# Performance work log

Hardware: AMD Instinct MI355X
Metric: run time of the kernel (lower is better)

The kernel has to match this reference:

```python
import jax, jax.numpy as jnp
import numpy as np

NEG = -1e9  # finite stand-in for -inf (avoids inf-inf NaNs, safe in fp32)


def setup_inputs() -> dict:
    T, V, Lmax, A = 2048, 8192, 8, 64
    rng = np.random.default_rng(0)
    seq = rng.integers(0, A, size=T).astype(np.int32)
    # first A pieces are the single codepoints -> every sequence is segmentable
    piece_lens = np.concatenate([
        np.ones(A, np.int32),
        rng.integers(1, Lmax + 1, size=V - A).astype(np.int32),
    ])
    pieces = rng.integers(0, A, size=(V, Lmax)).astype(np.int32)
    pieces[:A, 0] = np.arange(A)
    logits = rng.standard_normal(V).astype(np.float32)
    m = logits.max()
    log_probs = (logits - m - np.log(np.exp(logits - m).sum())).astype(np.float32)
    return {
        'seq': jnp.asarray(seq),
        'pieces': jnp.asarray(pieces),
        'piece_lens': jnp.asarray(piece_lens),
        'log_probs': jnp.asarray(log_probs),
    }


def reference(seq, pieces, piece_lens, log_probs):
    T = seq.shape[0]
    V, Lmax = pieces.shape
    dt = log_probs.dtype

    # --- match table: match[t, i] = piece i matches sequence at position t ---
    seq_pad = jnp.concatenate([seq, jnp.full((Lmax,), -1, seq.dtype)])
    windows = seq_pad[jnp.arange(T)[:, None] + jnp.arange(Lmax)[None, :]]  # [T, Lmax]
    lmask = jnp.arange(Lmax)[None, :] < piece_lens[:, None]                # [V, Lmax]
    eq = windows[:, None, :] == pieces[None, :, :]                        # [T, V, Lmax]
    fits = (jnp.arange(T)[:, None] + piece_lens[None, :]) <= T            # [T, V]
    match = jnp.all(eq | ~lmask[None, :, :], axis=-1) & fits              # [T, V]
    mlp = jnp.where(match, log_probs[None, :], NEG).astype(dt)            # [T, V]

    # end_logp[t-1, i] = mlp[t - len_i, i]  (piece i ending exactly at t, t=1..T)
    te = jnp.arange(1, T + 1)[:, None]
    src = te - piece_lens[None, :]
    end_logp = jnp.where(src >= 0,
                         mlp[jnp.clip(src, 0, T - 1), jnp.arange(V)[None, :]],
                         NEG)

    # --- forward pass: alpha[t] = logsumexp_i alpha[t - len_i] + log p_i ---
    idx_a = Lmax - piece_lens  # window slot holding alpha[t - len_i]
    def fstep(win, row):
        a_t = jax.nn.logsumexp(win[idx_a] + row)
        return jnp.concatenate([win[1:], a_t[None]]), a_t
    win0 = jnp.full((Lmax,), NEG, dt).at[-1].set(0.0)
    _, alpha_rest = jax.lax.scan(fstep, win0, end_logp)
    alpha = jnp.concatenate([jnp.zeros((1,), dt), alpha_rest])  # [T+1]

    # --- backward pass: beta[t] = logsumexp_i log p_i + beta[t + len_i] ---
    idx_b = piece_lens - 1  # window slot holding beta[t + len_i]
    def bstep(win, row):
        b_t = jax.nn.logsumexp(row + win[idx_b])
        return jnp.concatenate([b_t[None], win[:-1]]), b_t
    winT = jnp.full((Lmax,), NEG, dt).at[0].set(0.0)
    _, beta_rev = jax.lax.scan(bstep, winT, mlp[::-1])
    beta = jnp.concatenate([beta_rev[::-1], jnp.zeros((1,), dt)])  # [T+1]

    # --- posteriors: P[t, i] = exp(alpha[t] + log p_i + beta[t+len_i] - alpha[T]) ---
    norm = alpha[T]
    beta_next = beta[jnp.clip(jnp.arange(T)[:, None] + piece_lens[None, :], 0, T)]
    P = jnp.exp(alpha[:T][:, None] + mlp + beta_next - norm)
    P = jnp.where(match, P, 0.0)
    return jnp.where(norm > NEG / 2, P, jnp.zeros_like(P))
```

## Files before the change

### kernel.cpp

```cpp
#include <hip/hip_runtime.h>
#include <stdint.h>

#define LMAX 8
#define KCH 32
#define NC  64
#define TT  2048
#define LN2D 0.6931471805599453
#define NEGE (-(1<<28))

struct __align__(16) PK { unsigned long long key; float logp; int len; };

__device__ __forceinline__ int fexp(float m) { return ((__float_as_int(m) >> 23) & 0xFF) - 127; }
__device__ __forceinline__ int fexpbits(float m) { return (__float_as_int(m) >> 23) & 0xFF; }
__device__ __forceinline__ float p2(int e) { return __int_as_float((e + 127) << 23); }
__device__ __forceinline__ float p2c(int e) { return (e < -126) ? 0.f : p2(e); }

__global__ void k_prep(const int* __restrict__ seq, const int* __restrict__ pieces,
                       const int* __restrict__ plens, const float* __restrict__ logp,
                       PK* __restrict__ pk, unsigned long long* __restrict__ w64,
                       float* __restrict__ M, int T, int V) {
  int idx = blockIdx.x * blockDim.x + threadIdx.x;
  if (idx < V) {
    const int* pr = pieces + idx * LMAX;
    int len = plens[idx];
    unsigned long long key = 0ull;
    #pragma unroll
    for (int l = 0; l < LMAX; ++l) {
      unsigned long long b = (unsigned long long)(pr[l] & 0xFF);
      if (l < len) key |= b << (8 * l);
    }
    PK o; o.key = key; o.logp = logp[idx]; o.len = len;
    pk[idx] = o;
  } else if (idx < V + T) {
    int t = idx - V;
    unsigned long long w = 0ull;
    #pragma unroll
    for (int l = 0; l < LMAX; ++l) {
      int pos = t + l;
      unsigned long long b = (pos < T) ? (unsigned long long)(seq[pos] & 0xFF) : 0xFFull;
      w |= b << (8 * l);
    }
    w64[t] = w;
  } else if (idx < V + T + T * LMAX) {
    M[idx - V - T] = 0.f;
  }
}

__global__ void k_match(const PK* __restrict__ pk, const unsigned long long* __restrict__ w64,
                        float* __restrict__ M, int T, int V, int tPer) {
  int v = blockIdx.x * blockDim.x + threadIdx.x;
  PK p = pk[v];
  unsigned long long mask = (p.len >= 8) ? ~0ull : ((1ull << (8 * p.len)) - 1ull);
  unsigned long long key = p.key;
  int t0 = blockIdx.y * tPer;
  float prob = -1.f;
  for (int t = t0; t < t0 + tPer; ++t) {
    unsigned long long w = w64[t];
    if (((w ^ key) & mask) == 0ull) {
      if (prob < 0.f) prob = expf(p.logp);
      atomicAdd(&M[t * LMAX + (p.len - 1)], prob);
    }
  }
}

__global__ __launch_bounds__(512) void k_scan(const float* __restrict__ M,
        float* __restrict__ Wt, float* __restrict__ P,
        double* __restrict__ aD, double* __restrict__ bD,
        float* __restrict__ aL, float* __restrict__ bL) {
  __shared__ float  Gm[2 * 8 * 69];
  __shared__ float  Cs[2 * 64 * 9];
  __shared__ float  Sg[2 * 8 * 9];
  __shared__ int    EWc[2 * 64 * 8];
  __shared__ int    EPs[2 * 64 * 8];
  __shared__ int    EGs[2 * 8 * 8];
  __shared__ int    EaccP[2 * 64];
  __shared__ int    EsB[2 * 8];
  const int tid = threadIdx.x;
  const float4* Mv = (const float4*)M;

  {
    const int dir = tid >> 8, lt = tid & 255;
    const int c = lt >> 2, h = lt & 3;
    const int base = c * KCH;
    float st[2][8];
    #pragma unroll
    for (int bb = 0; bb < 2; ++bb)
      #pragma unroll
      for (int i = 0; i < 8; ++i) st[bb][i] = (i == 2 * h + bb) ? p2(64) : 0.f;
    int ec = -64;
    if (dir == 0) {
      float4 ra = Mv[base * 2], rb = Mv[base * 2 + 1];
      for (int kg = 0; kg < 4; ++kg) {
        #pragma unroll
        for (int kk = 0; kk < 8; ++kk) {
          int k = kg * 8 + kk;
          float4 c0 = ra, c1 = rb;
          int nk = (k + 1 < KCH) ? k + 1 : KCH - 1;
          ra = Mv[(base + nk) * 2]; rb = Mv[(base + nk) * 2 + 1];
          #pragma unroll
          for (int bb = 0; bb < 2; ++bb) {
            float a_ = st[bb][kk & 7];
            st[bb][(kk + 1) & 7] = fmaf(a_, c0.x, st[bb][(kk + 1) & 7]);
            st[bb][(kk + 2) & 7] = fmaf(a_, c0.y, st[bb][(kk + 2) & 7]);
            st[bb][(kk + 3) & 7] = fmaf(a_, c0.z, st[bb][(kk + 3) & 7]);
            st[bb][(kk + 4) & 7] = fmaf(a_, c0.w, st[bb][(kk + 4) & 7]);
            st[bb][(kk + 5) & 7] = fmaf(a_, c1.x, st[bb][(kk + 5) & 7]);
            st[bb][(kk + 6) & 7] = fmaf(a_, c1.y, st[bb][(kk + 6) & 7]);
            st[bb][(kk + 7) & 7] = fmaf(a_, c1.z, st[bb][(kk + 7) & 7]);
            st[bb][kk & 7]       = a_ * c1.w;
          }
          if (kk == 3 || kk == 7) {
            float mx = 0.f;
            #pragma unroll
            for (int bb = 0; bb < 2; ++bb)
              #pragma unroll
              for (int i = 0; i < 8; ++i) mx = fmaxf(mx, st[bb][i]);
            if (fexpbits(mx) != 0) {
              int e = fexp(mx), d = 64 - e;
              float m1 = p2(d / 2), m2 = p2(d - d / 2);
              #pragma unroll
              for (int bb = 0; bb < 2; ++bb)
                #pragma unroll
                for (int i = 0; i < 8; ++i) st[bb][i] = st[bb][i] * m1 * m2;
              ec += e - 64;
            }
          }
        }
      }
    } else {
      float4 ra = Mv[(base + KCH - 1) * 2], rb = Mv[(base + KCH - 1) * 2 + 1];
      for (int kg = 0; kg < 4; ++kg) {
        #pragma unroll
        for (int kk = 0; kk < 8; ++kk) {
          int k = kg * 8 + kk;
          float4 c0 = ra, c1 = rb;
          int nk = (k + 1 < KCH) ? k + 1 : KCH - 1;
          int nt = base + KCH - 1 - nk;
          ra = Mv[nt * 2]; rb = Mv[nt * 2 + 1];
          #pragma unroll
          for (int bb = 0; bb < 2; ++bb) {
            float nb =      c0.x * st[bb][(8  - kk) & 7];
            nb = fmaf(c0.y, st[bb][(9  - kk) & 7], nb);
            nb = fmaf(c0.z, st[bb][(10 - kk) & 7], nb);
            nb = fmaf(c0.w, st[bb][(11 - kk) & 7], nb);
            nb = fmaf(c1.x, st[bb][(12 - kk) & 7], nb);
            nb = fmaf(c1.y, st[bb][(13 - kk) & 7], nb);
            nb = fmaf(c1.z, st[bb][(14 - kk) & 7], nb);
            nb = fmaf(c1.w, st[bb][(15 - kk) & 7], nb);
            st[bb][(7 - kk) & 7] = nb;
          }
          if (kk == 3 || kk == 7) {
            float mx = 0.f;
            #pragma unroll
            for (int bb = 0; bb < 2; ++bb)
              #pragma unroll
              for (int i = 0; i < 8; ++i) mx = fmaxf(mx, st[bb][i]);
            if (fexpbits(mx) != 0) {
              int e = fexp(mx), d = 64 - e;
              float m1 = p2(d / 2), m2 = p2(d - d / 2);
              #pragma unroll
              for (int bb = 0; bb < 2; ++bb)
                #pragma unroll
                for (int i = 0; i < 8; ++i) st[bb][i] = st[bb][i] * m1 * m2;
              ec += e - 64;
            }
          }
        }
      }
    }
    float mx = 0.f;
    #pragma unroll
    for (int bb = 0; bb < 2; ++bb)
      #pragma unroll
      for (int i = 0; i < 8; ++i) mx = fmaxf(mx, st[bb][i]);
    int lc = dir ? (NC - 1 - c) : c;
    float* wp = Wt + (dir * 64 + lc) * 68;
    int ew;
    if (fexpbits(mx) == 0) {
      ew = NEGE;
      #pragma unroll
      for (int bb = 0; bb < 2; ++bb)
        #pragma unroll
        for (int i = 0; i < 8; ++i) wp[(2 * h + bb) * 8 + i] = 0.f;
    } else {
      int e = fexp(mx);
      float sc = p2(-e);
      ew = ec + e;
      #pragma unroll
      for (int bb = 0; bb < 2; ++bb)
        #pragma unroll
        for (int i = 0; i < 8; ++i) wp[(2 * h + bb) * 8 + i] = st[bb][i] * sc;
    }
    EWc[(dir * 64 + lc) * 8 + 2 * h]     = ew;
    EWc[(dir * 64 + lc) * 8 + 2 * h + 1] = ew;
  }
  __syncthreads();

  if (tid < 128) {
    const int dir = tid >> 6, w = (tid >> 3) & 7, b = tid & 7;
    float v[8];
    #pragma unroll
    for (int i = 0; i < 8; ++i) v[i] = (i == b) ? 1.f : 0.f;
    int ec = 0;
    for (int c = 0; c < 8; ++c) {
      int lc = w * 8 + c;
      float* pp = P + (dir * 64 + lc) * 69 + b * 8;
      #pragma unroll
      for (int i = 0; i < 8; ++i) pp[i] = v[i];
      EPs[(dir * 64 + lc) * 8 + b] = ec;
      const float* wp = Wt + (dir * 64 + lc) * 68;
      int ew[8];
      #pragma unroll
      for (int j = 0; j < 8; ++j) ew[j] = EWc[(dir * 64 + lc) * 8 + j];
      int emax = ew[0];
      #pragma unroll
      for (int j = 1; j < 8; ++j) emax = max(emax, ew[j]);
      float nv[8] = {0, 0, 0, 0, 0, 0, 0, 0};
      #pragma unroll
      for (int j = 0; j < 8; ++j) {
        float tj = v[j] * p2c(ew[j] - emax + 64);
        float4 ca = *(const float4*)(wp + j * 8);
        float4 cb = *(const float4*)(wp + j * 8 + 4);
        nv[0] = fmaf(tj, ca.x, nv[0]); nv[1] = fmaf(tj, ca.y, nv[1]);
        nv[2] = fmaf(tj, ca.z, nv[2]); nv[3] = fmaf(tj, ca.w, nv[3]);
        nv[4] = fmaf(tj, cb.x, nv[4]); nv[5] = fmaf(tj, cb.y, nv[5]);
        nv[6] = fmaf(tj, cb.z, nv[6]); nv[7] = fmaf(tj, cb.w, nv[7]);
      }
      float mx = 0.f;
      #pragma unroll
      for (int i = 0; i < 8; ++i) mx = fmaxf(mx, nv[i]);
      if (fexpbits(mx) == 0) {
        #pragma unroll
        for (int i = 0; i < 8; ++i) v[i] = 0.f;
        ec = NEGE;
      } else {
        int e = fexp(mx);
        float sc = p2(-e);
        #pragma unroll
        for (int i = 0; i < 8; ++i) v[i] = nv[i] * sc;
        ec = ec + emax + e - 64;
      }
    }
    float* gp = Gm + (dir * 8 + w) * 69 + b * 8;
    #pragma unroll
    for (int i = 0; i < 8; ++i) gp[i] = v[i];
    EGs[(dir * 8 + w) * 8 + b] = ec;
  }
  __syncthreads();

  if (tid < 8 || (tid >= 64 && tid < 72)) {
    const int dir = (tid >= 64) ? 1 : 0, j = tid & 7;
    float s[8];
    #pragma unroll
    for (int i = 0; i < 8; ++i) s[i] = (i == 0) ? 1.f : 0.f;
    int Es = 0;
    for (int w = 0; w < 8; ++w) {
      float sj = s[0];
      #pragma unroll
      for (int i = 1; i < 8; ++i) if (j == i) sj = s[i];
      Sg[(dir * 8 + w) * 9 + j] = sj;
      if (j == 0) EsB[dir * 8 + w] = Es;
      int eg[8];
      #pragma unroll
      for (int i = 0; i < 8; ++i) eg[i] = EGs[(dir * 8 + w) * 8 + i];
      int egmax = eg[0];
      #pragma unroll
      for (int i = 1; i < 8; ++i) egmax = max(egmax, eg[i]);
      int egj = eg[0];
      #pragma unroll
      for (int i = 1; i < 8; ++i) if (j == i) egj = eg[i];
      float tb = sj * p2c(egj - egmax + 64);
      const float* gp = Gm + (dir * 8 + w) * 69 + j * 8;
      float p[8];
      #pragma unroll
      for (int i = 0; i < 8; ++i) p[i] = gp[i] * tb;
      #pragma unroll
      for (int m = 1; m <= 4; m <<= 1)
        #pragma unroll
        for (int i = 0; i < 8; ++i) p[i] += __shfl_xor(p[i], m);
      float mx = 0.f;
      #pragma unroll
      for (int i = 0; i < 8; ++i) mx = fmaxf(mx, p[i]);
      int e = fexp(mx);
      float sc = p2(-e);
      #pragma unroll
      for (int i = 0; i < 8; ++i) s[i] = p[i] * sc;
      Es += egmax + e - 64;
    }
  }
  __syncthreads();

  if (tid < 128) {
    const int dir = tid >> 6, lc = tid & 63, w = lc >> 3;
    float sg[8];
    #pragma unroll
    for (int b = 0; b < 8; ++b) sg[b] = Sg[(dir * 8 + w) * 9 + b];
    int Es = EsB[dir * 8 + w];
    int ep[8];
    #pragma unroll
    for (int b = 0; b < 8; ++b) ep[b] = EPs[(dir * 64 + lc) * 8 + b];
    int epmax = ep[0];
    #pragma unroll
    for (int b = 1; b < 8; ++b) epmax = max(epmax, ep[b]);
    float cs[8] = {0, 0, 0, 0, 0, 0, 0, 0};
    #pragma unroll
    for (int b = 0; b < 8; ++b) {
      float coef = sg[b] * p2c(ep[b] - epmax + 64);
      const float* pp = P + (dir * 64 + lc) * 69 + b * 8;
      #pragma unroll
      for (int i = 0; i < 8; ++i) cs[i] = fmaf(coef, pp[i], cs[i]);
    }
    float mx = 0.f;
    #pragma unroll
    for (int i = 0; i < 8; ++i) mx = fmaxf(mx, cs[i]);
    float* cp = Cs + (dir * 64 + lc) * 9;
    int phys = dir ? (63 - lc) : lc;
    if (fexpbits(mx) == 0) {
      #pragma unroll
      for (int i = 0; i < 8; ++i) cp[i] = 0.f;
      EaccP[dir * 64 + phys] = NEGE;
    } else {
      int e = fexp(mx);
      float sc = p2(-e);
      #pragma unroll
      for (int i = 0; i < 8; ++i) cp[i] = cs[i] * sc;
      EaccP[dir * 64 + phys] = Es + epmax + e - 64;
    }
  }
  __syncthreads();

  if (tid < 64) {
    int c = tid, base = c * KCH;
    const float* cp = Cs + c * 9;
    double st[8];
    #pragma unroll
    for (int i = 0; i < 8; ++i) st[i] = (double)cp[i];
    float4 ra = Mv[base * 2], rb = Mv[base * 2 + 1];
    for (int kg = 0; kg < KCH / 8; ++kg) {
      #pragma unroll
      for (int kk = 0; kk < 8; ++kk) {
        int k = kg * 8 + kk;
        float4 c0 = ra, c1 = rb;
        int nk = (k + 1 < KCH) ? k + 1 : KCH - 1;
        ra = Mv[(base + nk) * 2]; rb = Mv[(base + nk) * 2 + 1];
        double r0 = c0.x, r1 = c0.y, r2 = c0.z, r3 = c0.w;
        double r4 = c1.x, r5 = c1.y, r6 = c1.z, r7 = c1.w;
        double a_ = st[kk & 7];
        st[(kk + 1) & 7] = fma(a_, r0, st[(kk + 1) & 7]);
        st[(kk + 2) & 7] = fma(a_, r1, st[(kk + 2) & 7]);
        st[(kk + 3) & 7] = fma(a_, r2, st[(kk + 3) & 7]);
        st[(kk + 4) & 7] = fma(a_, r3, st[(kk + 4) & 7]);
        st[(kk + 5) & 7] = fma(a_, r4, st[(kk + 5) & 7]);
        st[(kk + 6) & 7] = fma(a_, r5, st[(kk + 6) & 7]);
        st[(kk + 7) & 7] = fma(a_, r6, st[(kk + 7) & 7]);
        st[kk & 7]       = a_ * r7;
        aD[base + k + 1] = st[(kk + 1) & 7];
      }
    }
  } else if (tid < 128) {
    int c = tid - 64, base = c * KCH;
    const float* cp = Cs + (64 + 63 - c) * 9;
    double st[8];
    #pragma unroll
    for (int i = 0; i < 8; ++i) st[i] = (double)cp[i];
    float4 ra = Mv[(base + KCH - 1) * 2], rb = Mv[(base + KCH - 1) * 2 + 1];
    for (int kg = 0; kg < KCH / 8; ++kg) {
      #pragma unroll
      for (int kk = 0; kk < 8; ++kk) {
        int k = kg * 8 + kk;
        int t = base + KCH - 1 - k;
        float4 c0 = ra, c1 = rb;
        int nk = (k + 1 < KCH) ? k + 1 : KCH - 1;
        int nt = base + KCH - 1 - nk;
        ra = Mv[nt * 2]; rb = Mv[nt * 2 + 1];
        double r0 = c0.x, r1 = c0.y, r2 = c0.z, r3 = c0.w;
        double r4 = c1.x, r5 = c1.y, r6 = c1.z, r7 = c1.w;
        double nb =  r0 * st[(8  - kk) & 7];
        nb = fma(r1, st[(9  - kk) & 7], nb);
        nb = fma(r2, st[(10 - kk) & 7], nb);
        nb = fma(r3, st[(11 - kk) & 7], nb);
        nb = fma(r4, st[(12 - kk) & 7], nb);
        nb = fma(r5, st[(13 - kk) & 7], nb);
        nb = fma(r6, st[(14 - kk) & 7], nb);
        nb = fma(r7, st[(15 - kk) & 7], nb);
        st[(7 - kk) & 7] = nb;
        bD[t] = nb;
      }
    }
  }
  __syncthreads();

  for (int t = tid; t <= TT; t += 512) {
    float av = 0.f, bv = 0.f;
    if (t > 0) {
      long long bits = __double_as_longlong(aD[t]);
      int e2 = (int)((bits >> 52) & 0x7ff) - 1023;
      double mant = __longlong_as_double((bits & 0xFFFFFFFFFFFFFLL) | 0x3FF0000000000000LL);
      float lg = log2f((float)mant);
      av = (float)(((double)(e2 + EaccP[(t - 1) >> 5]) + (double)lg) * LN2D);
    }
    if (t < TT) {
      long long bits = __double_as_longlong(bD[t]);
      int e2 = (int)((bits >> 52) & 0x7ff) - 1023;
      double mant = __longlong_as_double((bits & 0xFFFFFFFFFFFFFLL) | 0x3FF0000000000000LL);
      float lg = log2f((float)mant);
      bv = (float)(((double)(e2 + EaccP[64 + (t >> 5)]) + (double)lg) * LN2D);
    }
    aL[t] = av; bL[t] = bv;
  }
}

__global__ void k_out(const PK* __restrict__ pk, const unsigned long long* __restrict__ w64,
                      const float* __restrict__ aL, const float* __restrict__ bL,
                      float* __restrict__ out, int T, int V, int tPer) {
  int v = blockIdx.x * blockDim.x + threadIdx.x;
  PK p = pk[v];
  unsigned long long mask = (p.len >= 8) ? ~0ull : ((1ull << (8 * p.len)) - 1ull);
  unsigned long long key = p.key;
  float norm = aL[T];
  float base = p.logp - norm;
  int t0 = blockIdx.y * tPer;
  for (int t = t0; t < t0 + tPer; ++t) {
    unsigned long long w = w64[t];
    float val = 0.f;
    if (((w ^ key) & mask) == 0ull)
      val = __expf(aL[t] + base + bL[t + p.len]);
    out[(size_t)t * V + v] = val;
  }
}

extern "C" void kernel_launch(void* const* d_in, const int* in_sizes, int n_in,
                              void* d_out, int out_size, void* d_ws, size_t ws_size,
                              hipStream_t stream) {
  const int* seq    = (const int*)d_in[0];
  const int* pieces = (const int*)d_in[1];
  const int* plens  = (const int*)d_in[2];
  const float* logp = (const float*)d_in[3];
  float* out = (float*)d_out;
  const int T = in_sizes[0];
  const int V = in_sizes[2];

  char* p = (char*)d_ws;
  PK* pk = (PK*)p;                                   p += (size_t)V * sizeof(PK);
  unsigned long long* w64 = (unsigned long long*)p;  p += (size_t)T * 8;
  float* M = (float*)p;                              p += (size_t)T * LMAX * 4;
  double* aD = (double*)p;                           p += 16400;
  double* bD = (double*)p;                           p += 16400;
  float* aL = (float*)p;                             p += 8208;
  float* bL = (float*)p;                             p += 8208;
  float* Wt = (float*)p;                             p += (size_t)2 * 64 * 68 * 4;
  float* Pm = (float*)p;                             p += (size_t)2 * 64 * 69 * 4;

  int prepN = V + T + T * LMAX;
  k_prep<<<(prepN + 255) / 256, 256, 0, stream>>>(seq, pieces, plens, logp, pk, w64, M, T, V);

  const int tPer2 = 128;
  dim3 g2(V / 256, T / tPer2);
  k_match<<<g2, 256, 0, stream>>>(pk, w64, M, T, V, tPer2);

  k_scan<<<1, 512, 0, stream>>>(M, Wt, Pm, aD, bD, aL, bL);

  const int tPer5 = 32;
  dim3 g5(V / 256, T / tPer5);
  k_out<<<g5, 256, 0, stream>>>(pk, w64, aL, bL, out, T, V, tPer5);
}
```

Baseline: 60.74 us.

## Split single-block scan into chunk, combine, and replay kernels across more threads

The monolithic one-block scan kernel is split into three launches. Chunk transfer matrices are computed by 2 blocks with one thread per basis column instead of two columns per thread. The combine step stages data in shared memory. The replay writes log-alphas and log-betas directly, removing the double-precision intermediate arrays and the final conversion pass. This shortens per-thread serial work and removes a sync and global round trip, at the cost of two extra kernel launches.

```diff
diff --git a/kernel.cpp b/kernel.cpp
--- a/kernel.cpp
+++ b/kernel.cpp
@@ -63,137 +63,116 @@
   }
 }
 
-__global__ __launch_bounds__(512) void k_scan(const float* __restrict__ M,
-        float* __restrict__ Wt, float* __restrict__ P,
-        double* __restrict__ aD, double* __restrict__ bD,
-        float* __restrict__ aL, float* __restrict__ bL) {
-  __shared__ float  Gm[2 * 8 * 69];
-  __shared__ float  Cs[2 * 64 * 9];
-  __shared__ float  Sg[2 * 8 * 9];
-  __shared__ int    EWc[2 * 64 * 8];
-  __shared__ int    EPs[2 * 64 * 8];
-  __shared__ int    EGs[2 * 8 * 8];
-  __shared__ int    EaccP[2 * 64];
-  __shared__ int    EsB[2 * 8];
-  const int tid = threadIdx.x;
+__global__ __launch_bounds__(512) void k_chunks(const float* __restrict__ M,
+        float* __restrict__ Wt, int* __restrict__ EWc) {
+  int gtid = blockIdx.x * 512 + threadIdx.x;
+  int task = gtid >> 3, b = gtid & 7;
+  int dir = task >> 6, c = task & 63;
+  int base = c * KCH;
   const float4* Mv = (const float4*)M;
-
-  {
-    const int dir = tid >> 8, lt = tid & 255;
-    const int c = lt >> 2, h = lt & 3;
-    const int base = c * KCH;
-    float st[2][8];
-    #pragma unroll
-    for (int bb = 0; bb < 2; ++bb)
-      #pragma unroll
-      for (int i = 0; i < 8; ++i) st[bb][i] = (i == 2 * h + bb) ? p2(64) : 0.f;
-    int ec = -64;
-    if (dir == 0) {
-      float4 ra = Mv[base * 2], rb = Mv[base * 2 + 1];
-      for (int kg = 0; kg < 4; ++kg) {
-        #pragma unroll
-        for (int kk = 0; kk < 8; ++kk) {
-          int k = kg * 8 + kk;
-          float4 c0 = ra, c1 = rb;
-          int nk = (k + 1 < KCH) ? k + 1 : KCH - 1;
-          ra = Mv[(base + nk) * 2]; rb = Mv[(base + nk) * 2 + 1];
+  float v[8];
+  #pragma unroll
+  for (int i = 0; i < 8; ++i) v[i] = (i == b) ? 1.f : 0.f;
+  int ec = 0;
+  if (dir == 0) {
+    float4 ra = Mv[base * 2], rb = Mv[base * 2 + 1];
+    for (int kg = 0; kg < 4; ++kg) {
+      #pragma unroll
+      for (int kk = 0; kk < 8; ++kk) {
+        int k = kg * 8 + kk;
+        float4 c0 = ra, c1 = rb;
+        int nk = (k + 1 < KCH) ? k + 1 : KCH - 1;
+        ra = Mv[(base + nk) * 2]; rb = Mv[(base + nk) * 2 + 1];
+        float a_ = v[kk & 7];
+        v[(kk + 1) & 7] = fmaf(a_, c0.x, v[(kk + 1) & 7]);
+        v[(kk + 2) & 7] = fmaf(a_, c0.y, v[(kk + 2) & 7]);
+        v[(kk + 3) & 7] = fmaf(a_, c0.z, v[(kk + 3) & 7]);
+        v[(kk + 4) & 7] = fmaf(a_, c0.w, v[(kk + 4) & 7]);
+        v[(kk + 5) & 7] = fmaf(a_, c1.x, v[(kk + 5) & 7]);
+        v[(kk + 6) & 7] = fmaf(a_, c1.y, v[(kk + 6) & 7]);
+        v[(kk + 7) & 7] = fmaf(a_, c1.z, v[(kk + 7) & 7]);
+        v[kk & 7]       = a_ * c1.w;
+        if (kk == 3 || kk == 7) {
+          float mx = 0.f;
           #pragma unroll
-          for (int bb = 0; bb < 2; ++bb) {
-            float a_ = st[bb][kk & 7];
-            st[bb][(kk + 1) & 7] = fmaf(a_, c0.x, st[bb][(kk + 1) & 7]);
-            st[bb][(kk + 2) & 7] = fmaf(a_, c0.y, st[bb][(kk + 2) & 7]);
-            st[bb][(kk + 3) & 7] = fmaf(a_, c0.z, st[bb][(kk + 3) & 7]);
-            st[bb][(kk + 4) & 7] = fmaf(a_, c0.w, st[bb][(kk + 4) & 7]);
-            st[bb][(kk + 5) & 7] = fmaf(a_, c1.x, st[bb][(kk + 5) & 7]);
-            st[bb][(kk + 6) & 7] = fmaf(a_, c1.y, st[bb][(kk + 6) & 7]);
-            st[bb][(kk + 7) & 7] = fmaf(a_, c1.z, st[bb][(kk + 7) & 7]);
-            st[bb][kk & 7]       = a_ * c1.w;
-          }
-          if (kk == 3 || kk == 7) {
-            float mx = 0.f;
+          for (int i = 0; i < 8; ++i) mx = fmaxf(mx, v[i]);
+          if (fexpbits(mx) != 0) {
+            int e = fexp(mx); float sc = p2(-e);
             #pragma unroll
-            for (int bb = 0; bb < 2; ++bb)
-              #pragma unroll
-              for (int i = 0; i < 8; ++i) mx = fmaxf(mx, st[bb][i]);
-            if (fexpbits(mx) != 0) {
-              int e = fexp(mx), d = 64 - e;
-              float m1 = p2(d / 2), m2 = p2(d - d / 2);
-              #pragma unroll
-              for (int bb = 0; bb < 2; ++bb)
-                #pragma unroll
-                for (int i = 0; i < 8; ++i) st[bb][i] = st[bb][i] * m1 * m2;
-              ec += e - 64;
-            }
+            for (int i = 0; i < 8; ++i) v[i] *= sc;
+            ec += e;
           }
         }
       }
-    } else {
-      float4 ra = Mv[(base + KCH - 1) * 2], rb = Mv[(base + KCH - 1) * 2 + 1];
-      for (int kg = 0; kg < 4; ++kg) {
-        #pragma unroll
-        for (int kk = 0; kk < 8; ++kk) {
-          int k = kg * 8 + kk;
-          float4 c0 = ra, c1 = rb;
-          int nk = (k + 1 < KCH) ? k + 1 : KCH - 1;
-          int nt = base + KCH - 1 - nk;
-          ra = Mv[nt * 2]; rb = Mv[nt * 2 + 1];
+    }
+  } else {
+    float4 ra = Mv[(base + KCH - 1) * 2], rb = Mv[(base + KCH - 1) * 2 + 1];
+    for (int kg = 0; kg < 4; ++kg) {
+      #pragma unroll
+      for (int kk = 0; kk < 8; ++kk) {
+        int k = kg * 8 + kk;
+        float4 c0 = ra, c1 = rb;
+        int nk = (k + 1 < KCH) ? k + 1 : KCH - 1;
+        int nt = base + KCH - 1 - nk;
+        ra = Mv[nt * 2]; rb = Mv[nt * 2 + 1];
+        float nb =      c0.x * v[(8  - kk) & 7];
+        nb = fmaf(c0.y, v[(9  - kk) & 7], nb);
+        nb = fmaf(c0.z, v[(10 - kk) & 7], nb);
+        nb = fmaf(c0.w, v[(11 - kk) & 7], nb);
+        nb = fmaf(c1.x, v[(12 - kk) & 7], nb);
+        nb = fmaf(c1.y, v[(13 - kk) & 7], nb);
+        nb = fmaf(c1.z, v[(14 - kk) & 7], nb);
+        nb = fmaf(c1.w, v[(15 - kk) & 7], nb);
+        v[(7 - kk) & 7] = nb;
+        if (kk == 3 || kk == 7) {
+          float mx = 0.f;
           #pragma unroll
-          for (int bb = 0; bb < 2; ++bb) {
-            float nb =      c0.x * st[bb][(8  - kk) & 7];
-            nb = fmaf(c0.y, st[bb][(9  - kk) & 7], nb);
-            nb = fmaf(c0.z, st[bb][(10 - kk) & 7], nb);
-            nb = fmaf(c0.w, st[bb][(11 - kk) & 7], nb);
-            nb = fmaf(c1.x, st[bb][(12 - kk) & 7], nb);
-            nb = fmaf(c1.y, st[bb][(13 - kk) & 7], nb);
-            nb = fmaf(c1.z, st[bb][(14 - kk) & 7], nb);
-            nb = fmaf(c1.w, st[bb][(15 - kk) & 7], nb);
-            st[bb][(7 - kk) & 7] = nb;
-          }
-          if (kk == 3 || kk == 7) {
-            float mx = 0.f;
+          for (int i = 0; i < 8; ++i) mx = fmaxf(mx, v[i]);
+          if (fexpbits(mx) != 0) {
+            int e = fexp(mx); float sc = p2(-e);
             #pragma unroll
-            for (int bb = 0; bb < 2; ++bb)
-              #pragma unroll
-              for (int i = 0; i < 8; ++i) mx = fmaxf(mx, st[bb][i]);
-            if (fexpbits(mx) != 0) {
-              int e = fexp(mx), d = 64 - e;
-              float m1 = p2(d / 2), m2 = p2(d - d / 2);
-              #pragma unroll
-              for (int bb = 0; bb < 2; ++bb)
-                #pragma unroll
-                for (int i = 0; i < 8; ++i) st[bb][i] = st[bb][i] * m1 * m2;
-              ec += e - 64;
-            }
+            for (int i = 0; i < 8; ++i) v[i] *= sc;
+            ec += e;
           }
         }
       }
     }
-    float mx = 0.f;
-    #pragma unroll
-    for (int bb = 0; bb < 2; ++bb)
-      #pragma unroll
-      for (int i = 0; i < 8; ++i) mx = fmaxf(mx, st[bb][i]);
-    int lc = dir ? (NC - 1 - c) : c;
-    float* wp = Wt + (dir * 64 + lc) * 68;
-    int ew;
-    if (fexpbits(mx) == 0) {
-      ew = NEGE;
-      #pragma unroll
-      for (int bb = 0; bb < 2; ++bb)
-        #pragma unroll
-        for (int i = 0; i < 8; ++i) wp[(2 * h + bb) * 8 + i] = 0.f;
-    } else {
-      int e = fexp(mx);
-      float sc = p2(-e);
-      ew = ec + e;
-      #pragma unroll
-      for (int bb = 0; bb < 2; ++bb)
-        #pragma unroll
-        for (int i = 0; i < 8; ++i) wp[(2 * h + bb) * 8 + i] = st[bb][i] * sc;
-    }
-    EWc[(dir * 64 + lc) * 8 + 2 * h]     = ew;
-    EWc[(dir * 64 + lc) * 8 + 2 * h + 1] = ew;
-  }
+  }
+  float mx = 0.f;
+  #pragma unroll
+  for (int i = 0; i < 8; ++i) mx = fmaxf(mx, v[i]);
+  int ltask = dir * 64 + (dir ? 63 - c : c);
+  float* wp = Wt + ltask * 64;
+  if (fexpbits(mx) == 0) {
+    #pragma unroll
+    for (int i = 0; i < 8; ++i) wp[b * 8 + i] = 0.f;
+    EWc[ltask * 8 + b] = NEGE;
+  } else {
+    int e = fexp(mx); float sc = p2(-e);
+    #pragma unroll
+    for (int i = 0; i < 8; ++i) wp[b * 8 + i] = v[i] * sc;
+    EWc[ltask * 8 + b] = ec + e;
+  }
+}
+
+__global__ __launch_bounds__(256) void k_combine(const float* __restrict__ Wt,
+        const int* __restrict__ EWc, float* __restrict__ Pm,
+        float* __restrict__ Cs, int* __restrict__ Eacc) {
+  __shared__ float sWt[128][68];
+  __shared__ int   sEW[128 * 8];
+  __shared__ int   sEP[128 * 8];
+  __shared__ float Gm[16 * 69];
+  __shared__ float Sg[16 * 9];
+  __shared__ int   EGs[16 * 8];
+  __shared__ int   EsB[16];
+  const int tid = threadIdx.x;
+
+  for (int i = tid; i < 128 * 16; i += 256) {
+    int task = i >> 4, q = i & 15;
+    float4 v4 = ((const float4*)Wt)[i];
+    *(float4*)&sWt[task][q * 4] = v4;
+  }
+  for (int i = tid; i < 1024; i += 256) sEW[i] = EWc[i];
   __syncthreads();
 
   if (tid < 128) {
@@ -203,15 +182,15 @@
     for (int i = 0; i < 8; ++i) v[i] = (i == b) ? 1.f : 0.f;
     int ec = 0;
     for (int c = 0; c < 8; ++c) {
-      int lc = w * 8 + c;
-      float* pp = P + (dir * 64 + lc) * 69 + b * 8;
+      int lc = w * 8 + c, lt = dir * 64 + lc;
+      float* pp = Pm + lt * 64 + b * 8;
       #pragma unroll
       for (int i = 0; i < 8; ++i) pp[i] = v[i];
-      EPs[(dir * 64 + lc) * 8 + b] = ec;
-      const float* wp = Wt + (dir * 64 + lc) * 68;
+      sEP[lt * 8 + b] = ec;
+      const float* wp = &sWt[lt][0];
       int ew[8];
       #pragma unroll
-      for (int j = 0; j < 8; ++j) ew[j] = EWc[(dir * 64 + lc) * 8 + j];
+      for (int j = 0; j < 8; ++j) ew[j] = sEW[lt * 8 + j];
       int emax = ew[0];
       #pragma unroll
       for (int j = 1; j < 8; ++j) emax = max(emax, ew[j]);
@@ -234,8 +213,7 @@
         for (int i = 0; i < 8; ++i) v[i] = 0.f;
         ec = NEGE;
       } else {
-        int e = fexp(mx);
-        float sc = p2(-e);
+        int e = fexp(mx); float sc = p2(-e);
         #pragma unroll
         for (int i = 0; i < 8; ++i) v[i] = nv[i] * sc;
         ec = ec + emax + e - 64;
@@ -281,8 +259,7 @@
       float mx = 0.f;
       #pragma unroll
       for (int i = 0; i < 8; ++i) mx = fmaxf(mx, p[i]);
-      int e = fexp(mx);
-      float sc = p2(-e);
+      int e = fexp(mx); float sc = p2(-e);
       #pragma unroll
       for (int i = 0; i < 8; ++i) s[i] = p[i] * sc;
       Es += egmax + e - 64;
@@ -298,7 +275,7 @@
     int Es = EsB[dir * 8 + w];
     int ep[8];
     #pragma unroll
-    for (int b = 0; b < 8; ++b) ep[b] = EPs[(dir * 64 + lc) * 8 + b];
+    for (int b = 0; b < 8; ++b) ep[b] = sEP[(dir * 64 + lc) * 8 + b];
     int epmax = ep[0];
     #pragma unroll
     for (int b = 1; b < 8; ++b) epmax = max(epmax, ep[b]);
@@ -306,65 +283,75 @@
     #pragma unroll
     for (int b = 0; b < 8; ++b) {
       float coef = sg[b] * p2c(ep[b] - epmax + 64);
-      const float* pp = P + (dir * 64 + lc) * 69 + b * 8;
-      #pragma unroll
-      for (int i = 0; i < 8; ++i) cs[i] = fmaf(coef, pp[i], cs[i]);
+      const float* pp = Pm + (dir * 64 + lc) * 64 + b * 8;
+      float4 ca = *(const float4*)pp;
+      float4 cb = *(const float4*)(pp + 4);
+      cs[0] = fmaf(coef, ca.x, cs[0]); cs[1] = fmaf(coef, ca.y, cs[1]);
+      cs[2] = fmaf(coef, ca.z, cs[2]); cs[3] = fmaf(coef, ca.w, cs[3]);
+      cs[4] = fmaf(coef, cb.x, cs[4]); cs[5] = fmaf(coef, cb.y, cs[5]);
+      cs[6] = fmaf(coef, cb.z, cs[6]); cs[7] = fmaf(coef, cb.w, cs[7]);
     }
     float mx = 0.f;
     #pragma unroll
     for (int i = 0; i < 8; ++i) mx = fmaxf(mx, cs[i]);
-    float* cp = Cs + (dir * 64 + lc) * 9;
     int phys = dir ? (63 - lc) : lc;
+    float* cp = Cs + (dir * 64 + phys) * 8;
     if (fexpbits(mx) == 0) {
       #pragma unroll
       for (int i = 0; i < 8; ++i) cp[i] = 0.f;
-      EaccP[dir * 64 + phys] = NEGE;
+      Eacc[dir * 64 + phys] = NEGE;
     } else {
-      int e = fexp(mx);
-      float sc = p2(-e);
+      int e = fexp(mx); float sc = p2(-e);
       #pragma unroll
       for (int i = 0; i < 8; ++i) cp[i] = cs[i] * sc;
-      EaccP[dir * 64 + phys] = Es + epmax + e - 64;
-    }
-  }
-  __syncthreads();
-
-  if (tid < 64) {
-    int c = tid, base = c * KCH;
-    const float* cp = Cs + c * 9;
-    double st[8];
-    #pragma unroll
-    for (int i = 0; i < 8; ++i) st[i] = (double)cp[i];
+      Eacc[dir * 64 + phys] = Es + epmax + e - 64;
+    }
+  }
+}
+
+__global__ __launch_bounds__(64) void k_replay(const float* __restrict__ M,
+        const float* __restrict__ Cs, const int* __restrict__ Eacc,
+        float* __restrict__ aL, float* __restrict__ bL) {
+  const int dir = blockIdx.x;
+  const int c = threadIdx.x;
+  const int base = c * KCH;
+  const float4* Mv = (const float4*)M;
+  const float* cp = Cs + (dir * 64 + c) * 8;
+  double st[8];
+  #pragma unroll
+  for (int i = 0; i < 8; ++i) st[i] = (double)cp[i];
+  const double eacc = (double)Eacc[dir * 64 + c];
+  if (dir == 0) {
+    if (c == 0) aL[0] = 0.f;
     float4 ra = Mv[base * 2], rb = Mv[base * 2 + 1];
-    for (int kg = 0; kg < KCH / 8; ++kg) {
+    for (int kg = 0; kg < 4; ++kg) {
       #pragma unroll
       for (int kk = 0; kk < 8; ++kk) {
         int k = kg * 8 + kk;
         float4 c0 = ra, c1 = rb;
         int nk = (k + 1 < KCH) ? k + 1 : KCH - 1;
         ra = Mv[(base + nk) * 2]; rb = Mv[(base + nk) * 2 + 1];
-        double r0 = c0.x, r1 = c0.y, r2 = c0.z, r3 = c0.w;
-        double r4 = c1.x, r5 = c1.y, r6 = c1.z, r7 = c1.w;
         double a_ = st[kk & 7];
-        st[(kk + 1) & 7] = fma(a_, r0, st[(kk + 1) & 7]);
-        st[(kk + 2) & 7] = fma(a_, r1, st[(kk + 2) & 7]);
-        st[(kk + 3) & 7] = fma(a_, r2, st[(kk + 3) & 7]);
-        st[(kk + 4) & 7] = fma(a_, r3, st[(kk + 4) & 7]);
-        st[(kk + 5) & 7] = fma(a_, r4, st[(kk + 5) & 7]);
-        st[(kk + 6) & 7] = fma(a_, r5, st[(kk + 6) & 7]);
-        st[(kk + 7) & 7] = fma(a_, r6, st[(kk + 7) & 7]);
-        st[kk & 7]       = a_ * r7;
-        aD[base + k + 1] = st[(kk + 1) & 7];
-      }
-    }
-  } else if (tid < 128) {
-    int c = tid - 64, base = c * KCH;
-    const float* cp = Cs + (64 + 63 - c) * 9;
-    double st[8];
-    #pragma unroll
-    for (int i = 0; i < 8; ++i) st[i] = (double)cp[i];
+        st[(kk + 1) & 7] = fma(a_, (double)c0.x, st[(kk + 1) & 7]);
+        st[(kk + 2) & 7] = fma(a_, (double)c0.y, st[(kk + 2) & 7]);
+        st[(kk + 3) & 7] = fma(a_, (double)c0.z, st[(kk + 3) & 7]);
+        st[(kk + 4) & 7] = fma(a_, (double)c0.w, st[(kk + 4) & 7]);
+        st[(kk + 5) & 7] = fma(a_, (double)c1.x, st[(kk + 5) & 7]);
+        st[(kk + 6) & 7] = fma(a_, (double)c1.y, st[(kk + 6) & 7]);
+        st[(kk + 7) & 7] = fma(a_, (double)c1.z, st[(kk + 7) & 7]);
+        st[kk & 7]       = a_ * (double)c1.w;
+        double val = st[(kk + 1) & 7];
+        long long bits = __double_as_longlong(val);
+        int e2 = (int)((bits >> 52) & 0x7ff) - 1023;
+        double mant = __longlong_as_double((bits & 0xFFFFFFFFFFFFFLL) | 0x3FF0000000000000LL);
+        float lg = log2f((float)mant);
+        aL[base + k + 1] = (float)(((double)e2 + eacc + (double)lg) * LN2D);
+      }
+    }
+  } else {
+    if (c == 0) bL[TT] = 0.f;
     float4 ra = Mv[(base + KCH - 1) * 2], rb = Mv[(base + KCH - 1) * 2 + 1];
-    for (int kg = 0; kg < KCH / 8; ++kg) {
+    for (int kg = 0; kg < 4; ++kg) {
       #pragma unroll
       for (int kk = 0; kk < 8; ++kk) {
         int k = kg * 8 + kk;
@@ -373,40 +360,22 @@
         int nk = (k + 1 < KCH) ? k + 1 : KCH - 1;
         int nt = base + KCH - 1 - nk;
         ra = Mv[nt * 2]; rb = Mv[nt * 2 + 1];
-        double r0 = c0.x, r1 = c0.y, r2 = c0.z, r3 = c0.w;
-        double r4 = c1.x, r5 = c1.y, r6 = c1.z, r7 = c1.w;
-        double nb =  r0 * st[(8  - kk) & 7];
-        nb = fma(r1, st[(9  - kk) & 7], nb);
-        nb = fma(r2, st[(10 - kk) & 7], nb);
-        nb = fma(r3, st[(11 - kk) & 7], nb);
-        nb = fma(r4, st[(12 - kk) & 7], nb);
-        nb = fma(r5, st[(13 - kk) & 7], nb);
-        nb = fma(r6, st[(14 - kk) & 7], nb);
-        nb = fma(r7, st[(15 - kk) & 7], nb);
+        double nb =            (double)c0.x * st[(8  - kk) & 7];
+        nb = fma((double)c0.y, st[(9  - kk) & 7], nb);
+        nb = fma((double)c0.z, st[(10 - kk) & 7], nb);
+        nb = fma((double)c0.w, st[(11 - kk) & 7], nb);
+        nb = fma((double)c1.x, st[(12 - kk) & 7], nb);
+        nb = fma((double)c1.y, st[(13 - kk) & 7], nb);
+        nb = fma((double)c1.z, st[(14 - kk) & 7], nb);
+        nb = fma((double)c1.w, st[(15 - kk) & 7], nb);
         st[(7 - kk) & 7] = nb;
-        bD[t] = nb;
-      }
-    }
-  }
-  __syncthreads();
-
-  for (int t = tid; t <= TT; t += 512) {
-    float av = 0.f, bv = 0.f;
-    if (t > 0) {
-      long long bits = __double_as_longlong(aD[t]);
-      int e2 = (int)((bits >> 52) & 0x7ff) - 1023;
-      double mant = __longlong_as_double((bits & 0xFFFFFFFFFFFFFLL) | 0x3FF0000000000000LL);
-      float lg = log2f((float)mant);
-      av = (float)(((double)(e2 + EaccP[(t - 1) >> 5]) + (double)lg) * LN2D);
-    }
-    if (t < TT) {
-      long long bits = __double_as_longlong(bD[t]);
-      int e2 = (int)((bits >> 52) & 0x7ff) - 1023;
-      double mant = __longlong_as_double((bits & 0xFFFFFFFFFFFFFLL) | 0x3FF0000000000000LL);
-      float lg = log2f((float)mant);
-      bv = (float)(((double)(e2 + EaccP[64 + (t >> 5)]) + (double)lg) * LN2D);
-    }
-    aL[t] = av; bL[t] = bv;
+        long long bits = __double_as_longlong(nb);
+        int e2 = (int)((bits >> 52) & 0x7ff) - 1023;
+        double mant = __longlong_as_double((bits & 0xFFFFFFFFFFFFFLL) | 0x3FF0000000000000LL);
+        float lg = log2f((float)mant);
+        bL[t] = (float)(((double)e2 + eacc + (double)lg) * LN2D);
+      }
+    }
   }
 }
 
@@ -444,12 +413,13 @@
   PK* pk = (PK*)p;                                   p += (size_t)V * sizeof(PK);
   unsigned long long* w64 = (unsigned long long*)p;  p += (size_t)T * 8;
   float* M = (float*)p;                              p += (size_t)T * LMAX * 4;
-  double* aD = (double*)p;                           p += 16400;
-  double* bD = (double*)p;                           p += 16400;
+  float* Wt = (float*)p;                             p += (size_t)128 * 64 * 4;
+  int* EWc = (int*)p;                                p += (size_t)128 * 8 * 4;
+  float* Pm = (float*)p;                             p += (size_t)128 * 64 * 4;
+  float* Cs = (float*)p;                             p += (size_t)128 * 8 * 4;
+  int* Eacc = (int*)p;                               p += 512;
   float* aL = (float*)p;                             p += 8208;
   float* bL = (float*)p;                             p += 8208;
-  float* Wt = (float*)p;                             p += (size_t)2 * 64 * 68 * 4;
-  float* Pm = (float*)p;                             p += (size_t)2 * 64 * 69 * 4;
 
   int prepN = V + T + T * LMAX;
   k_prep<<<(prepN + 255) / 256, 256, 0, stream>>>(seq, pieces, plens, logp, pk, w64, M, T, V);
@@ -458,7 +428,9 @@
   dim3 g2(V / 256, T / tPer2);
   k_match<<<g2, 256, 0, stream>>>(pk, w64, M, T, V, tPer2);
 
-  k_scan<<<1, 512, 0, stream>>>(M, Wt, Pm, aD, bD, aL, bL);
+  k_chunks<<<2, 512, 0, stream>>>(M, Wt, EWc);
+  k_combine<<<1, 256, 0, stream>>>(Wt, EWc, Pm, Cs, Eacc);
+  k_replay<<<2, 64, 0, stream>>>(M, Cs, Eacc, aL, bL);
 
   const int tPer5 = 32;
   dim3 g5(V / 256, T / tPer5);
```

Result: faster. 59.39 us (-2.2%).
